# Kernel tuning notes

Measured on AMD Instinct MI355X. Metric: run time of the kernel, lower is better.

The kernel has to match this reference:

```python
import jax, jax.numpy as jnp
import numpy as np

N_HEADS = 4
ATT_DIM = 640  # 10 * n_channels
SCALE = ATT_DIM ** (-0.5)


def setup_inputs() -> dict:
    key = jax.random.key(0)
    k1, k2, k3, k4, k5 = jax.random.split(key, 5)
    C, HpA = 64, N_HEADS * ATT_DIM  # 64, 2560
    x = jax.random.normal(k1, (8, C, 32, 32), dtype=jnp.float32)
    W_proj = jax.random.normal(k2, (C, 3 * HpA), dtype=jnp.float32) * (C ** -0.5)
    b_proj = jax.random.normal(k3, (3 * HpA,), dtype=jnp.float32) * 0.02
    W_out = jax.random.normal(k4, (HpA, C), dtype=jnp.float32) * (HpA ** -0.5)
    b_out = jax.random.normal(k5, (C,), dtype=jnp.float32) * 0.02
    return {"x": x, "t": 0, "W_proj": W_proj, "b_proj": b_proj, "W_out": W_out, "b_out": b_out}


def reference(x, t, W_proj, b_proj, W_out, b_out):
    del t  # unused, matches original signature
    b, c, w, h = x.shape
    seq = w * h
    xs = x.reshape(b, c, seq).transpose(0, 2, 1)  # [b, seq, C]
    proj = (xs @ W_proj + b_proj).reshape(b, seq, N_HEADS, 3 * ATT_DIM)
    q, k, v = jnp.split(proj, 3, axis=-1)  # each [b, seq, H, D]
    # scores [b, i, j, h]; NOTE softmax over axis=1 (queries), non-standard
    prod = jnp.einsum('bihd,bjhd->bijh', q, k) * SCALE
    soft = jax.nn.softmax(prod, axis=1)
    att = jnp.einsum('bijh,bjhd->bihd', soft, v)  # [b, seq, H, D]
    out = att.reshape(b, seq, N_HEADS * ATT_DIM) @ W_out + b_out  # [b, seq, C]
    out = out + xs
    return out.reshape(b, w, h, c).transpose(0, 3, 1, 2)
```

## Files before the change

### kernel.cpp

```cpp
#include <hip/hip_runtime.h>
#include <hip/hip_bf16.h>
#include <stdint.h>

typedef unsigned short u16;
typedef __attribute__((ext_vector_type(4))) float f32x4;
typedef __attribute__((ext_vector_type(8))) short bf16x8;

#define DEV __device__ __forceinline__

DEV float bf2f(u16 b){ unsigned u = ((unsigned)b) << 16; return __builtin_bit_cast(float, u); }
DEV u16 f2bf(float f){
  unsigned u = __builtin_bit_cast(unsigned, f);
  u += 0x7FFFu + ((u >> 16) & 1u);
  return (u16)(u >> 16);
}

DEV int xcd_swz(int nwg){
  const int bid = (int)blockIdx.x;
  return (bid & 7) * (nwg >> 3) + (bid >> 3);
}

DEV void stage_x64(const u16* srcbase, u16* dst, int tid){
  #pragma unroll
  for (int q = 0; q < 4; q++) {
    const int boff = q * 4096 + tid * 16;
    const int row = boff >> 7, slot = (boff & 127) >> 4;
    const int kk = (slot ^ (row & 7)) << 3;
    __builtin_amdgcn_global_load_lds(
        (const __attribute__((address_space(1))) void*)(srcbase + (long)row * 64 + kk),
        (__attribute__((address_space(3))) void*)(dst + (boff >> 1)), 16, 0, 0);
  }
}

DEV void tr_tile(float (*tile)[65], const float* src, u16* dst,
                 int R, int C, int r0, int c0)
{
  const int t = threadIdx.x;
  const int rr = t >> 2, cc = (t & 3) * 16;
  const float* sp = src + (long)(r0 + rr) * C + (c0 + cc);
  #pragma unroll
  for (int q = 0; q < 16; q++) tile[rr][cc + q] = sp[q];
  __syncthreads();
  u16* dp = dst + (long)(c0 + rr) * R + (r0 + cc);
  #pragma unroll
  for (int q = 0; q < 16; q++) dp[q] = f2bf(tile[cc + q][rr]);
}

__global__ __launch_bounds__(256) void k_misc(
    const float* __restrict__ x, const float* __restrict__ Wp,
    const float* __restrict__ Wo, const float* __restrict__ bp,
    u16* __restrict__ xt, u16* __restrict__ Wot, u16* __restrict__ Wpb,
    u16* __restrict__ xb, float* __restrict__ uh)
{
  __shared__ float tile[64][65];
  const int q = blockIdx.x;
  if (q < 240) {
    const long i = (long)q * 256 + threadIdx.x;
    const f32x4 a = *(const f32x4*)(Wp + i * 8);
    const f32x4 b = *(const f32x4*)(Wp + i * 8 + 4);
    bf16x8 r;
    #pragma unroll
    for (int e = 0; e < 4; e++){ r[e] = (short)f2bf(a[e]); r[e+4] = (short)f2bf(b[e]); }
    *(bf16x8*)(Wpb + i * 8) = r;
  } else if (q < 368) {
    const int p = q - 240, c0 = (p & 15) * 64, b = p >> 4;
    tr_tile(tile, x + (long)b * 65536, xt + (long)b * 65536, 64, 1024, 0, c0);
  } else if (q < 408) {
    const int p = q - 368;
    tr_tile(tile, Wo, Wot, 2560, 64, p * 64, 0);
  } else if (q < 472) {
    const int p = q - 408;
    const int wv = threadIdx.x >> 6, lane = threadIdx.x & 63;
    const int idx = p * 4 + wv;
    const int h = idx >> 6, c = idx & 63;
    const int qb = h * 1920, kb = qb + 640;
    const float* wrow = Wp + (long)c * 7680 + qb;
    float s = 0.f;
    #pragma unroll
    for (int d0 = 0; d0 < 640; d0 += 64)
      s += wrow[d0 + lane] * bp[kb + d0 + lane];
    #pragma unroll
    for (int off = 32; off; off >>= 1) s += __shfl_down(s, off);
    if (lane == 0) uh[idx] = s;
  } else {
    const int ch = (q - 472) * 256 + threadIdx.x;
    const int b = ch / 10240, rem = ch % 10240;
    const int row = rem >> 7, j8 = rem & 127;
    bf16x8 r;
    if (row < 64) {
      const float* sp = x + ((long)b * 64 + row) * 1024 + j8 * 8;
      const f32x4 a = *(const f32x4*)sp;
      const f32x4 bb = *(const f32x4*)(sp + 4);
      #pragma unroll
      for (int e = 0; e < 4; e++){ r[e] = (short)f2bf(a[e]); r[e+4] = (short)f2bf(bb[e]); }
    } else if (row == 64) {
      #pragma unroll
      for (int e = 0; e < 8; e++) r[e] = (short)0x3F80;
    } else {
      #pragma unroll
      for (int e = 0; e < 8; e++) r[e] = 0;
    }
    *(bf16x8*)(xb + ((long)b * 80 + row) * 1024 + j8 * 8) = r;
  }
}

__global__ __launch_bounds__(256) void k_nh(
    const u16* __restrict__ Wot, const float* __restrict__ bp,
    u16* __restrict__ MxT)
{
  const int wv = threadIdx.x >> 6, lane = threadIdx.x & 63;
  const int idx = blockIdx.x * 4 + wv;
  const int h = idx >> 6, cp = idx & 63;
  const u16* wr_ = Wot + (long)cp * 2560 + h * 640;
  const float* bv = bp + h * 1920 + 1280;
  float s = 0.f;
  #pragma unroll
  for (int d0 = 0; d0 < 640; d0 += 64)
    s += bf2f(wr_[d0 + lane]) * bv[d0 + lane];
  #pragma unroll
  for (int off = 32; off; off >>= 1) s += __shfl_down(s, off);
  if (lane == 0) MxT[cp * 320 + h * 80 + 64] = f2bf(s);
  if (lane >= 1 && lane < 16) MxT[cp * 320 + h * 80 + 64 + lane] = 0;
}

template<int BM, int BN, int BK, int WR, int WC, int MF, int NF>
DEV void gemm_nt(const u16* __restrict__ A, const u16* __restrict__ B,
                 int K, long lda, long ldb, int arow0, int brow0,
                 f32x4 (&acc)[MF][NF], u16* As, u16* Bs)
{
  const int tid  = threadIdx.x;
  const int lane = tid & 63;
  const int w    = tid >> 6;
  const int wr   = w / WC, wc = w % WC;
  constexpr int NT   = WR * WC * 64;
  constexpr int AISS = (BM * BK * 2) / (NT * 16);
  constexpr int BISS = (BN * BK * 2) / (NT * 16);
  constexpr int ABUF = BM * BK;
  constexpr int BBUF = BN * BK;

  #pragma unroll
  for (int m = 0; m < MF; m++)
    #pragma unroll
    for (int n = 0; n < NF; n++) acc[m][n] = f32x4{0.f, 0.f, 0.f, 0.f};

  const int frow = lane & 15;
  const int fs   = lane >> 4;

  auto stage = [&](int buf, int kt) {
    #pragma unroll
    for (int q = 0; q < AISS; q++) {
      const int boff = q * NT * 16 + tid * 16;
      const int row  = boff / (BK * 2);
      const int slot = (boff % (BK * 2)) >> 4;
      const int kk   = ((slot ^ (row & 7)) << 3);
      const u16* src = A + (long)(arow0 + row) * lda + kt + kk;
      __builtin_amdgcn_global_load_lds(
          (const __attribute__((address_space(1))) void*)src,
          (__attribute__((address_space(3))) void*)(As + buf * ABUF + (boff >> 1)), 16, 0, 0);
    }
    #pragma unroll
    for (int q = 0; q < BISS; q++) {
      const int boff = q * NT * 16 + tid * 16;
      const int row  = boff / (BK * 2);
      const int slot = (boff % (BK * 2)) >> 4;
      const int kk   = ((slot ^ (row & 7)) << 3);
      const u16* src = B + (long)(brow0 + row) * ldb + kt + kk;
      __builtin_amdgcn_global_load_lds(
          (const __attribute__((address_space(1))) void*)src,
          (__attribute__((address_space(3))) void*)(Bs + buf * BBUF + (boff >> 1)), 16, 0, 0);
    }
  };

  auto compute = [&](int buf) {
    __builtin_amdgcn_s_setprio(1);
    #pragma unroll
    for (int ks = 0; ks < BK / 32; ++ks) {
      bf16x8 af[MF], bfr[NF];
      #pragma unroll
      for (int m = 0; m < MF; m++) {
        const int row  = wr * (MF * 16) + m * 16 + frow;
        const int slot = (ks * 4 + fs) ^ (row & 7);
        af[m] = *(const bf16x8*)(As + buf * ABUF + row * BK + slot * 8);
      }
      #pragma unroll
      for (int n = 0; n < NF; n++) {
        const int row  = wc * (NF * 16) + n * 16 + frow;
        const int slot = (ks * 4 + fs) ^ (row & 7);
        bfr[n] = *(const bf16x8*)(Bs + buf * BBUF + row * BK + slot * 8);
      }
      #pragma unroll
      for (int m = 0; m < MF; m++)
        #pragma unroll
        for (int n = 0; n < NF; n++)
          acc[m][n] = __builtin_amdgcn_mfma_f32_16x16x32_bf16(af[m], bfr[n], acc[m][n], 0, 0, 0);
    }
    __builtin_amdgcn_s_setprio(0);
  };

  stage(0, 0);
  asm volatile("s_waitcnt vmcnt(0)" ::: "memory");
  __syncthreads();
  int cur = 0;
  for (int kt = BK; kt < K; kt += BK) {
    stage(cur ^ 1, kt);
    compute(cur);
    asm volatile("s_waitcnt vmcnt(0)" ::: "memory");
    __syncthreads();
    cur ^= 1;
  }
  compute(cur);
}

template<int MF, int NF, typename FV, typename FS>
DEV void epi_u16(u16* SH, FV&& fval, FS&& fstore)
{
  constexpr int RC = MF * 16, CC = NF * 16, CPR = NF * 2;
  const int lane = threadIdx.x & 63;
  const int w = threadIdx.x >> 6;
  u16* et = SH + w * (RC * CC);
  __syncthreads();
  #pragma unroll
  for (int m = 0; m < MF; m++)
    #pragma unroll
    for (int n = 0; n < NF; n++)
      #pragma unroll
      for (int j = 0; j < 4; j++) {
        const int row = m * 16 + (lane >> 4) * 4 + j;
        const int col = n * 16 + (lane & 15);
        et[row * CC + (((col >> 3) ^ row) & (CPR - 1)) * 8 + (col & 7)] =
            f2bf(fval(m, n, j, row, col));
      }
  constexpr int RPI = 64 / CPR;
  #pragma unroll
  for (int it = 0; it < RC / RPI; ++it) {
    const int row = it * RPI + lane / CPR;
    const int ch  = lane % CPR;
    bf16x8 v = *(const bf16x8*)(et + row * CC + ((ch ^ row) & (CPR - 1)) * 8);
    fstore(row, ch * 8, v);
  }
}

__global__ __launch_bounds__(256) void k_prep(
    const u16* __restrict__ Wpb, const u16* __restrict__ Wot,
    u16* __restrict__ Ahat, u16* __restrict__ MxT)
{
  __shared__ __align__(16) u16 SH[4 * 64 * 64];
  u16* As = SH; u16* Bs = SH + 2 * 64 * 64;
  const int q = blockIdx.x;
  const int w = threadIdx.x >> 6;
  const int wr = w >> 1, wc = w & 1;
  f32x4 acc[2][2];
  if (q < 4) {
    const int h = q;
    gemm_nt<64, 64, 64, 2, 2, 2, 2>(Wpb + h * 1920 + 640, Wpb + h * 1920, 640,
                                    7680, 7680, 0, 0, acc, As, Bs);
    u16* dst = Ahat + h * 4096;
    epi_u16<2, 2>(SH,
      [&](int m, int n, int j, int row, int col){ return acc[m][n][j]; },
      [&](int row, int c0, bf16x8 v){
        *(bf16x8*)(dst + (wr * 32 + row) * 64 + wc * 32 + c0) = v; });
  } else {
    const int h = q - 4;
    gemm_nt<64, 64, 64, 2, 2, 2, 2>(Wot + h * 640, Wpb + h * 1920 + 1280, 640,
                                    2560, 7680, 0, 0, acc, As, Bs);
    epi_u16<2, 2>(SH,
      [&](int m, int n, int j, int row, int col){ return acc[m][n][j]; },
      [&](int row, int c0, bf16x8 v){
        *(bf16x8*)(MxT + (long)(wr * 32 + row) * 320 + h * 80 + wc * 32 + c0) = v; });
  }
}

__global__ __launch_bounds__(256) void k_qkz(
    const u16* __restrict__ xt, const u16* __restrict__ Ahat,
    const float* __restrict__ uh, float* __restrict__ Z)
{
  __shared__ __align__(16) u16 XI[2][8192];
  __shared__ __align__(16) u16 AH[4096];
  __shared__ __align__(16) u16 XJ[8192];
  __shared__ __align__(16) u16 TT[8192];
  __shared__ float uts[128];
  __shared__ float uhl[64];
  __shared__ float Zs[2][128];
  const int tid = threadIdx.x, lane = tid & 63, w = tid >> 6;
  const int frow = lane & 15, fs = lane >> 4;
  const int wr = w >> 1, wc = w & 1;
  const int id = xcd_swz(256);
  const int bh = id >> 3, tj = id & 7;
  const int b = bh >> 2, h = bh & 3;
  const int j0 = b * 1024 + tj * 128;

  #pragma unroll
  for (int q = 0; q < 2; q++) {
    const int boff = q * 4096 + tid * 16;
    const int row = boff >> 7, slot = (boff & 127) >> 4;
    const int kk = (slot ^ (row & 7)) << 3;
    __builtin_amdgcn_global_load_lds(
        (const __attribute__((address_space(1))) void*)(Ahat + h * 4096 + row * 64 + kk),
        (__attribute__((address_space(3))) void*)(AH + (boff >> 1)), 16, 0, 0);
  }
  stage_x64(xt + (long)j0 * 64, XJ, tid);
  stage_x64(xt + (long)(b * 1024) * 64, XI[0], tid);
  if (tid < 64) uhl[tid] = uh[h * 64 + tid];
  asm volatile("s_waitcnt vmcnt(0)" ::: "memory");
  __syncthreads();

  float csum[4] = {0.f, 0.f, 0.f, 0.f};
  int cur = 0;
  for (int it = 0; it < 8; ++it) {
    if (it < 7) stage_x64(xt + (long)(b * 1024 + (it + 1) * 128) * 64, XI[cur ^ 1], tid);
    f32x4 acc1[4][2];
    #pragma unroll
    for (int m = 0; m < 4; m++)
      #pragma unroll
      for (int n = 0; n < 2; n++) acc1[m][n] = f32x4{0.f, 0.f, 0.f, 0.f};
    #pragma unroll
    for (int ks = 0; ks < 2; ks++) {
      bf16x8 af[4], bfr[2];
      #pragma unroll
      for (int m = 0; m < 4; m++) {
        const int row = wr * 64 + m * 16 + frow;
        af[m] = *(const bf16x8*)(XI[cur] + row * 64 + (((ks * 4 + fs) ^ (row & 7)) << 3));
      }
      #pragma unroll
      for (int n = 0; n < 2; n++) {
        const int row = wc * 32 + n * 16 + frow;
        bfr[n] = *(const bf16x8*)(AH + row * 64 + (((ks * 4 + fs) ^ (row & 7)) << 3));
      }
      #pragma unroll
      for (int m = 0; m < 4; m++)
        #pragma unroll
        for (int n = 0; n < 2; n++)
          acc1[m][n] = __builtin_amdgcn_mfma_f32_16x16x32_bf16(af[m], bfr[n], acc1[m][n], 0, 0, 0);
    }
    float su = 0.f;
    if (tid < 128) {
      #pragma unroll
      for (int s = 0; s < 8; s++) {
        bf16x8 v = *(const bf16x8*)(XI[cur] + tid * 64 + ((s ^ (tid & 7)) << 3));
        #pragma unroll
        for (int e = 0; e < 8; e++) su += bf2f((u16)v[e]) * uhl[s * 8 + e];
      }
    }
    __syncthreads();
    if (tid < 128) uts[tid] = su;
    #pragma unroll
    for (int m = 0; m < 4; m++)
      #pragma unroll
      for (int n = 0; n < 2; n++)
        #pragma unroll
        for (int j = 0; j < 4; j++) {
          const int row = wr * 64 + m * 16 + (lane >> 4) * 4 + j;
          const int col = wc * 32 + n * 16 + (lane & 15);
          TT[row * 64 + (((col >> 3) ^ (row & 7)) << 3) + (col & 7)] = f2bf(acc1[m][n][j]);
        }
    asm volatile("s_waitcnt vmcnt(0)" ::: "memory");
    __syncthreads();
    f32x4 sacc[4][4];
    #pragma unroll
    for (int m = 0; m < 4; m++)
      #pragma unroll
      for (int n = 0; n < 4; n++) sacc[m][n] = f32x4{0.f, 0.f, 0.f, 0.f};
    #pragma unroll
    for (int ks = 0; ks < 2; ks++) {
      bf16x8 af[4], bfr[4];
      #pragma unroll
      for (int m = 0; m < 4; m++) {
        const int row = wr * 64 + m * 16 + frow;
        af[m] = *(const bf16x8*)(TT + row * 64 + (((ks * 4 + fs) ^ (row & 7)) << 3));
      }
      #pragma unroll
      for (int n = 0; n < 4; n++) {
        const int row = wc * 64 + n * 16 + frow;
        bfr[n] = *(const bf16x8*)(XJ + row * 64 + (((ks * 4 + fs) ^ (row & 7)) << 3));
      }
      #pragma unroll
      for (int m = 0; m < 4; m++)
        #pragma unroll
        for (int n = 0; n < 4; n++)
          sacc[m][n] = __builtin_amdgcn_mfma_f32_16x16x32_bf16(af[m], bfr[n], sacc[m][n], 0, 0, 0);
    }
    #pragma unroll
    for (int m = 0; m < 4; m++)
      #pragma unroll
      for (int j = 0; j < 4; j++) {
        const float rv = uts[wr * 64 + m * 16 + (lane >> 4) * 4 + j];
        #pragma unroll
        for (int n = 0; n < 4; n++)
          csum[n] += __expf((sacc[m][n][j] + rv) * 0.03952847075210474f);
      }
    cur ^= 1;
  }
  #pragma unroll
  for (int n = 0; n < 4; n++) {
    csum[n] += __shfl_xor(csum[n], 16);
    csum[n] += __shfl_xor(csum[n], 32);
  }
  if ((lane >> 4) == 0) {
    #pragma unroll
    for (int n = 0; n < 4; n++) Zs[wr][wc * 64 + n * 16 + lane] = csum[n];
  }
  __syncthreads();
  if (tid < 128) Z[(long)bh * 1024 + tj * 128 + tid] = Zs[0][tid] + Zs[1][tid];
}

__global__ __launch_bounds__(256) void k_G(
    const u16* __restrict__ xt, const u16* __restrict__ xb,
    const u16* __restrict__ Ahat, const float* __restrict__ uh,
    const float* __restrict__ Z, u16* __restrict__ G)
{
  __shared__ __align__(16) u16 XIT[8192];
  __shared__ __align__(16) u16 AH[4096];
  __shared__ __align__(16) u16 XJ[2][8192];
  __shared__ __align__(16) u16 XB[10240];
  __shared__ __align__(16) u16 PT[16384];
  __shared__ float uts[128];
  __shared__ float uhl[64];
  __shared__ float rzs[128];
  const int tid = threadIdx.x, lane = tid & 63, w = tid >> 6;
  const int frow = lane & 15, fs = lane >> 4;
  const int wr = w >> 1, wc = w & 1;
  const int id = xcd_swz(256);
  const int bh = id >> 3, ti = id & 7;
  const int b = bh >> 2, h = bh & 3;
  const int i0 = b * 1024 + ti * 128;

  #pragma unroll
  for (int q = 0; q < 2; q++) {
    const int boff = q * 4096 + tid * 16;
    const int row = boff >> 7, slot = (boff & 127) >> 4;
    const int kk = (slot ^ (row & 7)) << 3;
    __builtin_amdgcn_global_load_lds(
        (const __attribute__((address_space(1))) void*)(Ahat + h * 4096 + row * 64 + kk),
        (__attribute__((address_space(3))) void*)(AH + (boff >> 1)), 16, 0, 0);
  }
  stage_x64(xt + (long)i0 * 64, XIT, tid);
  stage_x64(xt + (long)(b * 1024) * 64, XJ[0], tid);
  if (tid < 64) uhl[tid] = uh[h * 64 + tid];
  asm volatile("s_waitcnt vmcnt(0)" ::: "memory");
  __syncthreads();

  f32x4 acc1[4][2];
  #pragma unroll
  for (int m = 0; m < 4; m++)
    #pragma unroll
    for (int n = 0; n < 2; n++) acc1[m][n] = f32x4{0.f, 0.f, 0.f, 0.f};
  #pragma unroll
  for (int ks = 0; ks < 2; ks++) {
    bf16x8 af[4], bfr[2];
    #pragma unroll
    for (int m = 0; m < 4; m++) {
      const int row = wr * 64 + m * 16 + frow;
      af[m] = *(const bf16x8*)(XIT + row * 64 + (((ks * 4 + fs) ^ (row & 7)) << 3));
    }
    #pragma unroll
    for (int n = 0; n < 2; n++) {
      const int row = wc * 32 + n * 16 + frow;
      bfr[n] = *(const bf16x8*)(AH + row * 64 + (((ks * 4 + fs) ^ (row & 7)) << 3));
    }
    #pragma unroll
    for (int m = 0; m < 4; m++)
      #pragma unroll
      for (int n = 0; n < 2; n++)
        acc1[m][n] = __builtin_amdgcn_mfma_f32_16x16x32_bf16(af[m], bfr[n], acc1[m][n], 0, 0, 0);
  }
  float su = 0.f;
  if (tid < 128) {
    #pragma unroll
    for (int s = 0; s < 8; s++) {
      bf16x8 v = *(const bf16x8*)(XIT + tid * 64 + ((s ^ (tid & 7)) << 3));
      #pragma unroll
      for (int e = 0; e < 8; e++) su += bf2f((u16)v[e]) * uhl[s * 8 + e];
    }
  }
  __syncthreads();
  if (tid < 128) uts[tid] = su;
  #pragma unroll
  for (int m = 0; m < 4; m++)
    #pragma unroll
    for (int n = 0; n < 2; n++)
      #pragma unroll
      for (int j = 0; j < 4; j++) {
        const int row = wr * 64 + m * 16 + (lane >> 4) * 4 + j;
        const int col = wc * 32 + n * 16 + (lane & 15);
        XIT[row * 64 + (((col >> 3) ^ (row & 7)) << 3) + (col & 7)] = f2bf(acc1[m][n][j]);
      }
  __syncthreads();

  f32x4 gacc[2][5];
  #pragma unroll
  for (int m = 0; m < 2; m++)
    #pragma unroll
    for (int n = 0; n < 5; n++) gacc[m][n] = f32x4{0.f, 0.f, 0.f, 0.f};
  int cur = 0;
  for (int j = 0; j < 8; ++j) {
    #pragma unroll
    for (int q = 0; q < 5; q++) {
      const int boff = q * 4096 + tid * 16;
      const int c = boff >> 8, sl = (boff & 255) >> 4;
      const int kk = (sl ^ (c & 7)) << 3;
      __builtin_amdgcn_global_load_lds(
          (const __attribute__((address_space(1))) void*)(xb + ((long)b * 80 + c) * 1024 + j * 128 + kk),
          (__attribute__((address_space(3))) void*)(XB + (boff >> 1)), 16, 0, 0);
    }
    if (j < 7) stage_x64(xt + (long)(b * 1024 + (j + 1) * 128) * 64, XJ[cur ^ 1], tid);
    if (tid < 128) rzs[tid] = 1.0f / Z[(long)bh * 1024 + j * 128 + tid];
    f32x4 sacc[4][4];
    #pragma unroll
    for (int m = 0; m < 4; m++)
      #pragma unroll
      for (int n = 0; n < 4; n++) sacc[m][n] = f32x4{0.f, 0.f, 0.f, 0.f};
    #pragma unroll
    for (int ks = 0; ks < 2; ks++) {
      bf16x8 af[4], bfr[4];
      #pragma unroll
      for (int m = 0; m < 4; m++) {
        const int row = wr * 64 + m * 16 + frow;
        af[m] = *(const bf16x8*)(XIT + row * 64 + (((ks * 4 + fs) ^ (row & 7)) << 3));
      }
      #pragma unroll
      for (int n = 0; n < 4; n++) {
        const int row = wc * 64 + n * 16 + frow;
        bfr[n] = *(const bf16x8*)(XJ[cur] + row * 64 + (((ks * 4 + fs) ^ (row & 7)) << 3));
      }
      #pragma unroll
      for (int m = 0; m < 4; m++)
        #pragma unroll
        for (int n = 0; n < 4; n++)
          sacc[m][n] = __builtin_amdgcn_mfma_f32_16x16x32_bf16(af[m], bfr[n], sacc[m][n], 0, 0, 0);
    }
    __syncthreads();
    #pragma unroll
    for (int m = 0; m < 4; m++)
      #pragma unroll
      for (int jj = 0; jj < 4; jj++) {
        const int row = wr * 64 + m * 16 + (lane >> 4) * 4 + jj;
        const float rv = uts[row];
        #pragma unroll
        for (int n = 0; n < 4; n++) {
          const int col = wc * 64 + n * 16 + (lane & 15);
          const float p = __expf((sacc[m][n][jj] + rv) * 0.03952847075210474f) * rzs[col];
          PT[row * 128 + (((col >> 3) ^ (row & 7)) << 3) + (col & 7)] = f2bf(p);
        }
      }
    asm volatile("s_waitcnt vmcnt(0)" ::: "memory");
    __syncthreads();
    #pragma unroll
    for (int ks = 0; ks < 4; ks++) {
      bf16x8 af2[2], bfr2[5];
      #pragma unroll
      for (int m = 0; m < 2; m++) {
        const int row = w * 32 + m * 16 + frow;
        af2[m] = *(const bf16x8*)(PT + row * 128 + (((ks * 4 + fs) ^ (row & 7)) << 3));
      }
      #pragma unroll
      for (int n = 0; n < 5; n++) {
        const int rc = n * 16 + frow;
        bfr2[n] = *(const bf16x8*)(XB + rc * 128 + (((ks * 4 + fs) ^ (rc & 7)) << 3));
      }
      #pragma unroll
      for (int m = 0; m < 2; m++)
        #pragma unroll
        for (int n = 0; n < 5; n++)
          gacc[m][n] = __builtin_amdgcn_mfma_f32_16x16x32_bf16(af2[m], bfr2[n], gacc[m][n], 0, 0, 0);
    }
    __syncthreads();
    cur ^= 1;
  }
  #pragma unroll
  for (int m = 0; m < 2; m++)
    #pragma unroll
    for (int n = 0; n < 5; n++)
      #pragma unroll
      for (int jj = 0; jj < 4; jj++) {
        const int row = w * 32 + m * 16 + (lane >> 4) * 4 + jj;
        const int col = n * 16 + (lane & 15);
        PT[row * 80 + col] = f2bf(gacc[m][n][jj]);
      }
  __syncthreads();
  #pragma unroll
  for (int it = 0; it < 5; ++it) {
    const int task = it * 256 + tid;
    const int row = task / 10, ch = task % 10;
    bf16x8 v = *(const bf16x8*)(PT + row * 80 + ch * 8);
    *(bf16x8*)(G + (long)(i0 + row) * 320 + h * 80 + ch * 8) = v;
  }
}

__global__ __launch_bounds__(256) void k_out(
    const u16* __restrict__ G, const u16* __restrict__ MxT,
    const float* __restrict__ bo, const float* __restrict__ x, float* __restrict__ out)
{
  __shared__ __align__(16) u16 SH[2 * 128 * 64 + 2 * 64 * 64];
  u16* As = SH; u16* Bs = SH + 2 * 128 * 64;
  f32x4 acc[2][4];
  gemm_nt<128, 64, 64, 4, 1, 2, 4>(G, MxT, 320, 320, 320,
                                   blockIdx.x * 128, 0, acc, As, Bs);
  const int lane = threadIdx.x & 63;
  const int wr = threadIdx.x >> 6;
  float* etf = (float*)SH;
  __syncthreads();
  #pragma unroll
  for (int m = 0; m < 2; m++)
    #pragma unroll
    for (int n = 0; n < 4; n++)
      #pragma unroll
      for (int j = 0; j < 4; j++) {
        const int sl = wr * 32 + m * 16 + (lane >> 4) * 4 + j;
        const int c  = n * 16 + (lane & 15);
        etf[c * 132 + sl] = acc[m][n][j];
      }
  __syncthreads();
  const int b = blockIdx.x >> 3, s0 = (blockIdx.x & 7) * 128;
  #pragma unroll
  for (int it = 0; it < 8; ++it) {
    const int task = it * 256 + threadIdx.x;
    const int c = task >> 5, q = (task & 31) * 4;
    const float bias = bo[c];
    f32x4 v = *(const f32x4*)(etf + c * 132 + q);
    const long xi = ((long)(b * 64 + c) << 10) + s0 + q;
    const f32x4 xv = *(const f32x4*)(x + xi);
    #pragma unroll
    for (int e = 0; e < 4; e++) v[e] += bias + xv[e];
    *(f32x4*)(out + xi) = v;
  }
}

extern "C" void kernel_launch(void* const* d_in, const int* in_sizes, int n_in,
                              void* d_out, int out_size, void* d_ws, size_t ws_size,
                              hipStream_t stream)
{
  (void)in_sizes; (void)n_in; (void)out_size; (void)ws_size;
  const float* x  = (const float*)d_in[0];
  const float* Wp = (const float*)d_in[2];
  const float* bp = (const float*)d_in[3];
  const float* Wo = (const float*)d_in[4];
  const float* bo = (const float*)d_in[5];
  float* out = (float*)d_out;

  char* w8 = (char*)d_ws;
  u16*   xt   = (u16*)(w8 + 0L);
  u16*   xb   = (u16*)(w8 + 1048576L);
  u16*   Wot  = (u16*)(w8 + 2359296L);
  u16*   Wpb  = (u16*)(w8 + 2686976L);
  u16*   Ahat = (u16*)(w8 + 3670016L);
  u16*   MxT  = (u16*)(w8 + 3702784L);
  float* uh   = (float*)(w8 + 3743744L);
  float* Z    = (float*)(w8 + 3744768L);
  u16*   G    = (u16*)(w8 + 3875840L);

  k_misc<<<792, 256, 0, stream>>>(x, Wp, Wo, bp, xt, Wot, Wpb, xb, uh);
  k_nh  <<<64,  256, 0, stream>>>(Wot, bp, MxT);
  k_prep<<<8,   256, 0, stream>>>(Wpb, Wot, Ahat, MxT);
  k_qkz <<<256, 256, 0, stream>>>(xt, Ahat, uh, Z);
  k_G   <<<256, 256, 0, stream>>>(xt, xb, Ahat, uh, Z, G);
  k_out <<<64,  256, 0, stream>>>(G, MxT, bo, x, out);
}
```

Before: 76.74 us.

## Fuse weight prep GEMMs and bias fold into single misc kernel

Merges k_nh and k_prep into k_misc. The per-head Ahat and MxT products are now computed straight from the fp32 weights, converting to bf16 while staging into shared memory, so the intermediate bf16 copies of W_proj and W_out no longer need to be written and read back. This removes two kernel launches and their serialization. In exchange, eight long serial GEMM blocks now sit inside the large misc grid. A single block handles the bias fold with a scalar loop over 640 elements, which may become the critical path of the launch.

Result: slower. 86.63 us (+12.9%).

```diff
diff --git a/kernel.cpp b/kernel.cpp
--- a/kernel.cpp
+++ b/kernel.cpp
@@ -20,15 +20,20 @@
   return (bid & 7) * (nwg >> 3) + (bid >> 3);
 }
 
+DEV void gld16(const u16* src, u16* dst){
+  __builtin_amdgcn_global_load_lds(
+      (const __attribute__((address_space(1))) void*)src,
+      (__attribute__((address_space(3))) void*)dst, 16, 0, 0);
+}
+
+template<int NTH>
 DEV void stage_x64(const u16* srcbase, u16* dst, int tid){
   #pragma unroll
-  for (int q = 0; q < 4; q++) {
-    const int boff = q * 4096 + tid * 16;
+  for (int q = 0; q < 16384 / (NTH * 16); q++) {
+    const int boff = q * NTH * 16 + tid * 16;
     const int row = boff >> 7, slot = (boff & 127) >> 4;
     const int kk = (slot ^ (row & 7)) << 3;
-    __builtin_amdgcn_global_load_lds(
-        (const __attribute__((address_space(1))) void*)(srcbase + (long)row * 64 + kk),
-        (__attribute__((address_space(3))) void*)(dst + (boff >> 1)), 16, 0, 0);
+    gld16(srcbase + (long)row * 64 + kk, dst + (boff >> 1));
   }
 }
 
@@ -46,44 +51,135 @@
   for (int q = 0; q < 16; q++) dp[q] = f2bf(tile[cc + q][rr]);
 }
 
+template<int MF, int NF, typename FV, typename FS>
+DEV void epi_u16(u16* SH, FV&& fval, FS&& fstore)
+{
+  constexpr int RC = MF * 16, CC = NF * 16, CPR = NF * 2;
+  const int lane = threadIdx.x & 63;
+  const int w = threadIdx.x >> 6;
+  u16* et = SH + w * (RC * CC);
+  __syncthreads();
+  #pragma unroll
+  for (int m = 0; m < MF; m++)
+    #pragma unroll
+    for (int n = 0; n < NF; n++)
+      #pragma unroll
+      for (int j = 0; j < 4; j++) {
+        const int row = m * 16 + (lane >> 4) * 4 + j;
+        const int col = n * 16 + (lane & 15);
+        et[row * CC + (((col >> 3) ^ row) & (CPR - 1)) * 8 + (col & 7)] =
+            f2bf(fval(m, n, j, row, col));
+      }
+  constexpr int RPI = 64 / CPR;
+  #pragma unroll
+  for (int it = 0; it < RC / RPI; ++it) {
+    const int row = it * RPI + lane / CPR;
+    const int ch  = lane % CPR;
+    bf16x8 v = *(const bf16x8*)(et + row * CC + ((ch ^ row) & (CPR - 1)) * 8);
+    fstore(row, ch * 8, v);
+  }
+}
+
 __global__ __launch_bounds__(256) void k_misc(
     const float* __restrict__ x, const float* __restrict__ Wp,
     const float* __restrict__ Wo, const float* __restrict__ bp,
-    u16* __restrict__ xt, u16* __restrict__ Wot, u16* __restrict__ Wpb,
-    u16* __restrict__ xb, float* __restrict__ uh)
+    u16* __restrict__ xt, u16* __restrict__ xb,
+    float* __restrict__ uh, u16* __restrict__ Ahat, u16* __restrict__ MxT)
 {
   __shared__ float tile[64][65];
+  __shared__ __align__(16) u16 PA[4096];
+  __shared__ __align__(16) u16 PB[4096];
   const int q = blockIdx.x;
-  if (q < 240) {
-    const long i = (long)q * 256 + threadIdx.x;
-    const f32x4 a = *(const f32x4*)(Wp + i * 8);
-    const f32x4 b = *(const f32x4*)(Wp + i * 8 + 4);
-    bf16x8 r;
-    #pragma unroll
-    for (int e = 0; e < 4; e++){ r[e] = (short)f2bf(a[e]); r[e+4] = (short)f2bf(b[e]); }
-    *(bf16x8*)(Wpb + i * 8) = r;
-  } else if (q < 368) {
-    const int p = q - 240, c0 = (p & 15) * 64, b = p >> 4;
+  const int tid = threadIdx.x;
+  if (q < 8) {
+    const int h = q & 3;
+    const bool isA = q < 4;
+    const int lane = tid & 63, w = tid >> 6;
+    const int wr = w >> 1, wc = w & 1;
+    const int frow = lane & 15, fs = lane >> 4;
+    const int qb = h * 1920, kb = qb + 640, vb = qb + 1280;
+    f32x4 acc[2][2];
+    #pragma unroll
+    for (int m = 0; m < 2; m++)
+      #pragma unroll
+      for (int n = 0; n < 2; n++) acc[m][n] = f32x4{0.f, 0.f, 0.f, 0.f};
+    for (int kt = 0; kt < 640; kt += 64) {
+      __syncthreads();
+      if (isA) {
+        #pragma unroll
+        for (int rnd = 0; rnd < 4; rnd++) {
+          const int idx = rnd * 1024 + tid * 4;
+          const int row = idx >> 6, c4 = idx & 63;
+          const f32x4 v = *(const f32x4*)(Wp + (long)row * 7680 + kb + kt + c4);
+          uint2 pk;
+          pk.x = (unsigned)f2bf(v[0]) | ((unsigned)f2bf(v[1]) << 16);
+          pk.y = (unsigned)f2bf(v[2]) | ((unsigned)f2bf(v[3]) << 16);
+          *(uint2*)(PA + row * 64 + (((c4 >> 3) ^ (row & 7)) << 3) + (c4 & 4)) = pk;
+        }
+      } else {
+        #pragma unroll
+        for (int rnd = 0; rnd < 4; rnd++) {
+          const int idx = rnd * 1024 + tid * 4;
+          const int d = idx >> 6, c4 = idx & 63;
+          const f32x4 v = *(const f32x4*)(Wo + (long)(h * 640 + kt + d) * 64 + c4);
+          #pragma unroll
+          for (int e = 0; e < 4; e++) {
+            const int cp = c4 + e;
+            PA[cp * 64 + (((d >> 3) ^ (cp & 7)) << 3) + (d & 7)] = f2bf(v[e]);
+          }
+        }
+      }
+      {
+        const int base = isA ? qb : vb;
+        #pragma unroll
+        for (int rnd = 0; rnd < 4; rnd++) {
+          const int idx = rnd * 1024 + tid * 4;
+          const int row = idx >> 6, c4 = idx & 63;
+          const f32x4 v = *(const f32x4*)(Wp + (long)row * 7680 + base + kt + c4);
+          uint2 pk;
+          pk.x = (unsigned)f2bf(v[0]) | ((unsigned)f2bf(v[1]) << 16);
+          pk.y = (unsigned)f2bf(v[2]) | ((unsigned)f2bf(v[3]) << 16);
+          *(uint2*)(PB + row * 64 + (((c4 >> 3) ^ (row & 7)) << 3) + (c4 & 4)) = pk;
+        }
+      }
+      __syncthreads();
+      #pragma unroll
+      for (int ks = 0; ks < 2; ks++) {
+        bf16x8 af[2], bfr[2];
+        #pragma unroll
+        for (int m = 0; m < 2; m++) {
+          const int row = wr * 32 + m * 16 + frow;
+          af[m] = *(const bf16x8*)(PA + row * 64 + (((ks * 4 + fs) ^ (row & 7)) << 3));
+        }
+        #pragma unroll
+        for (int n = 0; n < 2; n++) {
+          const int row = wc * 32 + n * 16 + frow;
+          bfr[n] = *(const bf16x8*)(PB + row * 64 + (((ks * 4 + fs) ^ (row & 7)) << 3));
+        }
+        #pragma unroll
+        for (int m = 0; m < 2; m++)
+          #pragma unroll
+          for (int n = 0; n < 2; n++)
+            acc[m][n] = __builtin_amdgcn_mfma_f32_16x16x32_bf16(af[m], bfr[n], acc[m][n], 0, 0, 0);
+      }
+    }
+    if (isA) {
+      u16* dst = Ahat + h * 4096;
+      epi_u16<2, 2>(PA,
+        [&](int m, int n, int j, int row, int col){ return acc[m][n][j]; },
+        [&](int row, int c0, bf16x8 v){
+          *(bf16x8*)(dst + (wr * 32 + row) * 64 + wc * 32 + c0) = v; });
+    } else {
+      epi_u16<2, 2>(PA,
+        [&](int m, int n, int j, int row, int col){ return acc[m][n][j]; },
+        [&](int row, int c0, bf16x8 v){
+          *(bf16x8*)(MxT + (long)(wr * 32 + row) * 320 + h * 80 + wc * 32 + c0) = v; });
+    }
+  } else if (q < 136) {
+    const int p = q - 8, c0 = (p & 15) * 64, b = p >> 4;
     tr_tile(tile, x + (long)b * 65536, xt + (long)b * 65536, 64, 1024, 0, c0);
-  } else if (q < 408) {
-    const int p = q - 368;
-    tr_tile(tile, Wo, Wot, 2560, 64, p * 64, 0);
-  } else if (q < 472) {
-    const int p = q - 408;
-    const int wv = threadIdx.x >> 6, lane = threadIdx.x & 63;
-    const int idx = p * 4 + wv;
-    const int h = idx >> 6, c = idx & 63;
-    const int qb = h * 1920, kb = qb + 640;
-    const float* wrow = Wp + (long)c * 7680 + qb;
-    float s = 0.f;
-    #pragma unroll
-    for (int d0 = 0; d0 < 640; d0 += 64)
-      s += wrow[d0 + lane] * bp[kb + d0 + lane];
-    #pragma unroll
-    for (int off = 32; off; off >>= 1) s += __shfl_down(s, off);
-    if (lane == 0) uh[idx] = s;
-  } else {
-    const int ch = (q - 472) * 256 + threadIdx.x;
+  } else if (q < 456) {
+    const int ch = (q - 136) * 256 + tid;
     const int b = ch / 10240, rem = ch % 10240;
     const int row = rem >> 7, j8 = rem & 127;
     bf16x8 r;
@@ -101,172 +197,30 @@
       for (int e = 0; e < 8; e++) r[e] = 0;
     }
     *(bf16x8*)(xb + ((long)b * 80 + row) * 1024 + j8 * 8) = r;
-  }
-}
-
-__global__ __launch_bounds__(256) void k_nh(
-    const u16* __restrict__ Wot, const float* __restrict__ bp,
-    u16* __restrict__ MxT)
-{
-  const int wv = threadIdx.x >> 6, lane = threadIdx.x & 63;
-  const int idx = blockIdx.x * 4 + wv;
-  const int h = idx >> 6, cp = idx & 63;
-  const u16* wr_ = Wot + (long)cp * 2560 + h * 640;
-  const float* bv = bp + h * 1920 + 1280;
-  float s = 0.f;
-  #pragma unroll
-  for (int d0 = 0; d0 < 640; d0 += 64)
-    s += bf2f(wr_[d0 + lane]) * bv[d0 + lane];
-  #pragma unroll
-  for (int off = 32; off; off >>= 1) s += __shfl_down(s, off);
-  if (lane == 0) MxT[cp * 320 + h * 80 + 64] = f2bf(s);
-  if (lane >= 1 && lane < 16) MxT[cp * 320 + h * 80 + 64 + lane] = 0;
-}
-
-template<int BM, int BN, int BK, int WR, int WC, int MF, int NF>
-DEV void gemm_nt(const u16* __restrict__ A, const u16* __restrict__ B,
-                 int K, long lda, long ldb, int arow0, int brow0,
-                 f32x4 (&acc)[MF][NF], u16* As, u16* Bs)
-{
-  const int tid  = threadIdx.x;
-  const int lane = tid & 63;
-  const int w    = tid >> 6;
-  const int wr   = w / WC, wc = w % WC;
-  constexpr int NT   = WR * WC * 64;
-  constexpr int AISS = (BM * BK * 2) / (NT * 16);
-  constexpr int BISS = (BN * BK * 2) / (NT * 16);
-  constexpr int ABUF = BM * BK;
-  constexpr int BBUF = BN * BK;
-
-  #pragma unroll
-  for (int m = 0; m < MF; m++)
-    #pragma unroll
-    for (int n = 0; n < NF; n++) acc[m][n] = f32x4{0.f, 0.f, 0.f, 0.f};
-
-  const int frow = lane & 15;
-  const int fs   = lane >> 4;
-
-  auto stage = [&](int buf, int kt) {
-    #pragma unroll
-    for (int q = 0; q < AISS; q++) {
-      const int boff = q * NT * 16 + tid * 16;
-      const int row  = boff / (BK * 2);
-      const int slot = (boff % (BK * 2)) >> 4;
-      const int kk   = ((slot ^ (row & 7)) << 3);
-      const u16* src = A + (long)(arow0 + row) * lda + kt + kk;
-      __builtin_amdgcn_global_load_lds(
-          (const __attribute__((address_space(1))) void*)src,
-          (__attribute__((address_space(3))) void*)(As + buf * ABUF + (boff >> 1)), 16, 0, 0);
-    }
-    #pragma unroll
-    for (int q = 0; q < BISS; q++) {
-      const int boff = q * NT * 16 + tid * 16;
-      const int row  = boff / (BK * 2);
-      const int slot = (boff % (BK * 2)) >> 4;
-      const int kk   = ((slot ^ (row & 7)) << 3);
-      const u16* src = B + (long)(brow0 + row) * ldb + kt + kk;
-      __builtin_amdgcn_global_load_lds(
-          (const __attribute__((address_space(1))) void*)src,
-          (__attribute__((address_space(3))) void*)(Bs + buf * BBUF + (boff >> 1)), 16, 0, 0);
-    }
-  };
-
-  auto compute = [&](int buf) {
-    __builtin_amdgcn_s_setprio(1);
-    #pragma unroll
-    for (int ks = 0; ks < BK / 32; ++ks) {
-      bf16x8 af[MF], bfr[NF];
-      #pragma unroll
-      for (int m = 0; m < MF; m++) {
-        const int row  = wr * (MF * 16) + m * 16 + frow;
-        const int slot = (ks * 4 + fs) ^ (row & 7);
-        af[m] = *(const bf16x8*)(As + buf * ABUF + row * BK + slot * 8);
-      }
-      #pragma unroll
-      for (int n = 0; n < NF; n++) {
-        const int row  = wc * (NF * 16) + n * 16 + frow;
-        const int slot = (ks * 4 + fs) ^ (row & 7);
-        bfr[n] = *(const bf16x8*)(Bs + buf * BBUF + row * BK + slot * 8);
-      }
-      #pragma unroll
-      for (int m = 0; m < MF; m++)
-        #pragma unroll
-        for (int n = 0; n < NF; n++)
-          acc[m][n] = __builtin_amdgcn_mfma_f32_16x16x32_bf16(af[m], bfr[n], acc[m][n], 0, 0, 0);
-    }
-    __builtin_amdgcn_s_setprio(0);
-  };
-
-  stage(0, 0);
-  asm volatile("s_waitcnt vmcnt(0)" ::: "memory");
-  __syncthreads();
-  int cur = 0;
-  for (int kt = BK; kt < K; kt += BK) {
-    stage(cur ^ 1, kt);
-    compute(cur);
-    asm volatile("s_waitcnt vmcnt(0)" ::: "memory");
-    __syncthreads();
-    cur ^= 1;
-  }
-  compute(cur);
-}
-
-template<int MF, int NF, typename FV, typename FS>
-DEV void epi_u16(u16* SH, FV&& fval, FS&& fstore)
-{
-  constexpr int RC = MF * 16, CC = NF * 16, CPR = NF * 2;
-  const int lane = threadIdx.x & 63;
-  const int w = threadIdx.x >> 6;
-  u16* et = SH + w * (RC * CC);
-  __syncthreads();
-  #pragma unroll
-  for (int m = 0; m < MF; m++)
-    #pragma unroll
-    for (int n = 0; n < NF; n++)
-      #pragma unroll
-      for (int j = 0; j < 4; j++) {
-        const int row = m * 16 + (lane >> 4) * 4 + j;
-        const int col = n * 16 + (lane & 15);
-        et[row * CC + (((col >> 3) ^ row) & (CPR - 1)) * 8 + (col & 7)] =
-            f2bf(fval(m, n, j, row, col));
-      }
-  constexpr int RPI = 64 / CPR;
-  #pragma unroll
-  for (int it = 0; it < RC / RPI; ++it) {
-    const int row = it * RPI + lane / CPR;
-    const int ch  = lane % CPR;
-    bf16x8 v = *(const bf16x8*)(et + row * CC + ((ch ^ row) & (CPR - 1)) * 8);
-    fstore(row, ch * 8, v);
-  }
-}
-
-__global__ __launch_bounds__(256) void k_prep(
-    const u16* __restrict__ Wpb, const u16* __restrict__ Wot,
-    u16* __restrict__ Ahat, u16* __restrict__ MxT)
-{
-  __shared__ __align__(16) u16 SH[4 * 64 * 64];
-  u16* As = SH; u16* Bs = SH + 2 * 64 * 64;
-  const int q = blockIdx.x;
-  const int w = threadIdx.x >> 6;
-  const int wr = w >> 1, wc = w & 1;
-  f32x4 acc[2][2];
-  if (q < 4) {
-    const int h = q;
-    gemm_nt<64, 64, 64, 2, 2, 2, 2>(Wpb + h * 1920 + 640, Wpb + h * 1920, 640,
-                                    7680, 7680, 0, 0, acc, As, Bs);
-    u16* dst = Ahat + h * 4096;
-    epi_u16<2, 2>(SH,
-      [&](int m, int n, int j, int row, int col){ return acc[m][n][j]; },
-      [&](int row, int c0, bf16x8 v){
-        *(bf16x8*)(dst + (wr * 32 + row) * 64 + wc * 32 + c0) = v; });
+  } else if (q < 520) {
+    const int p = q - 456;
+    const int wv = tid >> 6, lane = tid & 63;
+    const int idx = p * 4 + wv;
+    const int h = idx >> 6, c = idx & 63;
+    const int qb = h * 1920, kb = qb + 640;
+    const float* wrow = Wp + (long)c * 7680 + qb;
+    float s = 0.f;
+    #pragma unroll
+    for (int d0 = 0; d0 < 640; d0 += 64)
+      s += wrow[d0 + lane] * bp[kb + d0 + lane];
+    #pragma unroll
+    for (int off = 32; off; off >>= 1) s += __shfl_down(s, off);
+    if (lane == 0) uh[idx] = s;
   } else {
-    const int h = q - 4;
-    gemm_nt<64, 64, 64, 2, 2, 2, 2>(Wot + h * 640, Wpb + h * 1920 + 1280, 640,
-                                    2560, 7680, 0, 0, acc, As, Bs);
-    epi_u16<2, 2>(SH,
-      [&](int m, int n, int j, int row, int col){ return acc[m][n][j]; },
-      [&](int row, int c0, bf16x8 v){
-        *(bf16x8*)(MxT + (long)(wr * 32 + row) * 320 + h * 80 + wc * 32 + c0) = v; });
+    const int wv = tid >> 6, lane = tid & 63;
+    const float* bv = bp + wv * 1920 + 1280;
+    float s = 0.f;
+    #pragma unroll 8
+    for (int d = 0; d < 640; d++)
+      s += Wo[(long)(wv * 640 + d) * 64 + lane] * bv[d];
+    MxT[lane * 320 + wv * 80 + 64] = f2bf(s);
+    #pragma unroll
+    for (int e = 1; e < 16; e++) MxT[lane * 320 + wv * 80 + 64 + e] = 0;
   }
 }
 
@@ -294,12 +248,10 @@
     const int boff = q * 4096 + tid * 16;
     const int row = boff >> 7, slot = (boff & 127) >> 4;
     const int kk = (slot ^ (row & 7)) << 3;
-    __builtin_amdgcn_global_load_lds(
-        (const __attribute__((address_space(1))) void*)(Ahat + h * 4096 + row * 64 + kk),
-        (__attribute__((address_space(3))) void*)(AH + (boff >> 1)), 16, 0, 0);
-  }
-  stage_x64(xt + (long)j0 * 64, XJ, tid);
-  stage_x64(xt + (long)(b * 1024) * 64, XI[0], tid);
+    gld16(Ahat + h * 4096 + row * 64 + kk, AH + (boff >> 1));
+  }
+  stage_x64<256>(xt + (long)j0 * 64, XJ, tid);
+  stage_x64<256>(xt + (long)(b * 1024) * 64, XI[0], tid);
   if (tid < 64) uhl[tid] = uh[h * 64 + tid];
   asm volatile("s_waitcnt vmcnt(0)" ::: "memory");
   __syncthreads();
@@ -307,7 +259,7 @@
   float csum[4] = {0.f, 0.f, 0.f, 0.f};
   int cur = 0;
   for (int it = 0; it < 8; ++it) {
-    if (it < 7) stage_x64(xt + (long)(b * 1024 + (it + 1) * 128) * 64, XI[cur ^ 1], tid);
+    if (it < 7) stage_x64<256>(xt + (long)(b * 1024 + (it + 1) * 128) * 64, XI[cur ^ 1], tid);
     f32x4 acc1[4][2];
     #pragma unroll
     for (int m = 0; m < 4; m++)
@@ -429,12 +381,10 @@
     const int boff = q * 4096 + tid * 16;
     const int row = boff >> 7, slot = (boff & 127) >> 4;
     const int kk = (slot ^ (row & 7)) << 3;
-    __builtin_amdgcn_global_load_lds(
-        (const __attribute__((address_space(1))) void*)(Ahat + h * 4096 + row * 64 + kk),
-        (__attribute__((address_space(3))) void*)(AH + (boff >> 1)), 16, 0, 0);
-  }
-  stage_x64(xt + (long)i0 * 64, XIT, tid);
-  stage_x64(xt + (long)(b * 1024) * 64, XJ[0], tid);
+    gld16(Ahat + h * 4096 + row * 64 + kk, AH + (boff >> 1));
+  }
+  stage_x64<256>(xt + (long)i0 * 64, XIT, tid);
+  stage_x64<256>(xt + (long)(b * 1024) * 64, XJ[0], tid);
   if (tid < 64) uhl[tid] = uh[h * 64 + tid];
   asm volatile("s_waitcnt vmcnt(0)" ::: "memory");
   __syncthreads();
@@ -498,11 +448,9 @@
       const int boff = q * 4096 + tid * 16;
       const int c = boff >> 8, sl = (boff & 255) >> 4;
       const int kk = (sl ^ (c & 7)) << 3;
-      __builtin_amdgcn_global_load_lds(
-          (const __attribute__((address_space(1))) void*)(xb + ((long)b * 80 + c) * 1024 + j * 128 + kk),
-          (__attribute__((address_space(3))) void*)(XB + (boff >> 1)), 16, 0, 0);
-    }
-    if (j < 7) stage_x64(xt + (long)(b * 1024 + (j + 1) * 128) * 64, XJ[cur ^ 1], tid);
+      gld16(xb + ((long)b * 80 + c) * 1024 + j * 128 + kk, XB + (boff >> 1));
+    }
+    if (j < 7) stage_x64<256>(xt + (long)(b * 1024 + (j + 1) * 128) * 64, XJ[cur ^ 1], tid);
     if (tid < 128) rzs[tid] = 1.0f / Z[(long)bh * 1024 + j * 128 + tid];
     f32x4 sacc[4][4];
     #pragma unroll
@@ -584,6 +532,88 @@
     bf16x8 v = *(const bf16x8*)(PT + row * 80 + ch * 8);
     *(bf16x8*)(G + (long)(i0 + row) * 320 + h * 80 + ch * 8) = v;
   }
+}
+
+template<int BM, int BN, int BK, int WR, int WC, int MF, int NF>
+DEV void gemm_nt(const u16* __restrict__ A, const u16* __restrict__ B,
+                 int K, long lda, long ldb, int arow0, int brow0,
+                 f32x4 (&acc)[MF][NF], u16* As, u16* Bs)
+{
+  const int tid  = threadIdx.x;
+  const int lane = tid & 63;
+  const int w    = tid >> 6;
+  const int wr   = w / WC, wc = w % WC;
+  constexpr int NT   = WR * WC * 64;
+  constexpr int AISS = (BM * BK * 2) / (NT * 16);
+  constexpr int BISS = (BN * BK * 2) / (NT * 16);
+  constexpr int ABUF = BM * BK;
+  constexpr int BBUF = BN * BK;
+
+  #pragma unroll
+  for (int m = 0; m < MF; m++)
+    #pragma unroll
+    for (int n = 0; n < NF; n++) acc[m][n] = f32x4{0.f, 0.f, 0.f, 0.f};
+
+  const int frow = lane & 15;
+  const int fs   = lane >> 4;
+
+  auto stage = [&](int buf, int kt) {
+    #pragma unroll
+    for (int q = 0; q < AISS; q++) {
+      const int boff = q * NT * 16 + tid * 16;
+      const int row  = boff / (BK * 2);
+      const int slot = (boff % (BK * 2)) >> 4;
+      const int kk   = ((slot ^ (row & 7)) << 3);
+      gld16(A + (long)(arow0 + row) * lda + kt + kk, As + buf * ABUF + (boff >> 1));
+    }
+    #pragma unroll
+    for (int q = 0; q < BISS; q++) {
+      const int boff = q * NT * 16 + tid * 16;
+      const int row  = boff / (BK * 2);
+      const int slot = (boff % (BK * 2)) >> 4;
+      const int kk   = ((slot ^ (row & 7)) << 3);
+      gld16(B + (long)(brow0 + row) * ldb + kt + kk, Bs + buf * BBUF + (boff >> 1));
+    }
+  };
+
+  auto compute = [&](int buf) {
+    __builtin_amdgcn_s_setprio(1);
+    #pragma unroll
+    for (int ks = 0; ks < BK / 32; ++ks) {
+      bf16x8 af[MF], bfr[NF];
+      #pragma unroll
+      for (int m = 0; m < MF; m++) {
+        const int row  = wr * (MF * 16) + m * 16 + frow;
+        const int slot = (ks * 4 + fs) ^ (row & 7);
+        af[m] = *(const bf16x8*)(As + buf * ABUF + row * BK + slot * 8);
+      }
+      #pragma unroll
+      for (int n = 0; n < NF; n++) {
+        const int row  = wc * (NF * 16) + n * 16 + frow;
+        const int slot = (ks * 4 + fs) ^ (row & 7);
+        bfr[n] = *(const bf16x8*)(Bs + buf * BBUF + row * BK + slot * 8);
+      }
+      #pragma unroll
+      for (int m = 0; m < MF; m++)
+        #pragma unroll
+        for (int n = 0; n < NF; n++)
+          acc[m][n] = __builtin_amdgcn_mfma_f32_16x16x32_bf16(af[m], bfr[n], acc[m][n], 0, 0, 0);
+    }
+    __builtin_amdgcn_s_setprio(0);
+  };
+
+  stage(0, 0);
+  asm volatile("s_waitcnt vmcnt(0)" ::: "memory");
+  __syncthreads();
+  int cur = 0;
+  for (int kt = BK; kt < K; kt += BK) {
+    stage(cur ^ 1, kt);
+    compute(cur);
+    asm volatile("s_waitcnt vmcnt(0)" ::: "memory");
+    __syncthreads();
+    cur ^= 1;
+  }
+  compute(cur);
 }
 
 __global__ __launch_bounds__(256) void k_out(
@@ -640,17 +670,13 @@
   char* w8 = (char*)d_ws;
   u16*   xt   = (u16*)(w8 + 0L);
   u16*   xb   = (u16*)(w8 + 1048576L);
-  u16*   Wot  = (u16*)(w8 + 2359296L);
-  u16*   Wpb  = (u16*)(w8 + 2686976L);
-  u16*   Ahat = (u16*)(w8 + 3670016L);
-  u16*   MxT  = (u16*)(w8 + 3702784L);
-  float* uh   = (float*)(w8 + 3743744L);
-  float* Z    = (float*)(w8 + 3744768L);
-  u16*   G    = (u16*)(w8 + 3875840L);
-
-  k_misc<<<792, 256, 0, stream>>>(x, Wp, Wo, bp, xt, Wot, Wpb, xb, uh);
-  k_nh  <<<64,  256, 0, stream>>>(Wot, bp, MxT);
-  k_prep<<<8,   256, 0, stream>>>(Wpb, Wot, Ahat, MxT);
+  u16*   Ahat = (u16*)(w8 + 2359296L);
+  u16*   MxT  = (u16*)(w8 + 2392064L);
+  float* uh   = (float*)(w8 + 2433024L);
+  float* Z    = (float*)(w8 + 2434048L);
+  u16*   G    = (u16*)(w8 + 2565120L);
+
+  k_misc<<<521, 256, 0, stream>>>(x, Wp, Wo, bp, xt, xb, uh, Ahat, MxT);
   k_qkz <<<256, 256, 0, stream>>>(xt, Ahat, uh, Z);
   k_G   <<<256, 256, 0, stream>>>(xt, xb, Ahat, uh, Z, G);
   k_out <<<64,  256, 0, stream>>>(G, MxT, bo, x, out);
```
